# Kernel tuning notes

Hardware: AMD Instinct MI355X
Metric: run time of the kernel (lower is better)

The kernel has to match this reference:

```python
import jax, jax.numpy as jnp
import numpy as np

BN_EPS = 1e-5
L2_EPS = 1e-12  # F.normalize eps
K = 9           # kernel_size (dilation=1 so effective k = 9)
GROUPS = 4      # hard-coded groups in MRConv2d


def setup_inputs() -> dict:
    key = jax.random.key(0)
    k1, k2, k3 = jax.random.split(key, 3)
    B, C, H, W = 32, 192, 28, 28
    Cout = 384
    x = jax.random.normal(k1, (B, C, H, W), jnp.float32)
    # Conv2d(2C, Cout, 1, groups=4) weight is [Cout, 2C//4, 1, 1]; store as [Cout, 2C//4]
    fan_in = 2 * C // GROUPS
    conv_w = jax.random.normal(k2, (Cout, fan_in), jnp.float32) * np.sqrt(2.0 / fan_in)
    conv_b = jax.random.normal(k3, (Cout,), jnp.float32) * 0.05
    gamma = jnp.ones((Cout,), jnp.float32)
    beta = jnp.zeros((Cout,), jnp.float32)
    return {"x": x, "conv_w": conv_w, "conv_b": conv_b, "gamma": gamma, "beta": beta}


def _knn_idx(xf, k):
    """xf: (B, C, N) -> nn_idx: (B, N, k) via L2-normalized pairwise distance + topk."""
    xn = xf / jnp.maximum(jnp.linalg.norm(xf, axis=1, keepdims=True), L2_EPS)
    xt = xn.transpose(0, 2, 1)                       # (B, N, C)
    sq = jnp.sum(xt * xt, axis=-1, keepdims=True)    # (B, N, 1)
    inner = jnp.einsum('bnc,bmc->bnm', xt, xt)       # (B, N, N)
    dist = sq - 2.0 * inner + sq.transpose(0, 2, 1)
    _, nn_idx = jax.lax.top_k(-dist, k)              # (B, N, k)
    return nn_idx


def _forward(x, conv_w, conv_b, gamma, beta):
    B, C, H, W = x.shape
    N = H * W
    xf = x.reshape(B, C, N)
    # KNN graph built on detached features (torch: no_grad + x.detach for y when r=1)
    y = jax.lax.stop_gradient(xf)
    nn_idx = _knn_idx(y, K)                                            # (B, N, K)
    # gather neighbor features: xj[b,c,n,kk] = y[b,c,nn_idx[b,n,kk]]
    xj = jax.vmap(lambda yb, ib: yb[:, ib])(y, nn_idx)                 # (B, C, N, K)
    # max-relative: max_k (x_j - x_i); center gather of edge_index[1] is just xf
    rel = jnp.max(xj - xf[:, :, :, None], axis=-1)                     # (B, C, N)
    # cat([x.unsqueeze(2), rel.unsqueeze(2)], dim=2).reshape(B, 2C, N): channel-interleaved
    h = jnp.stack([xf, rel], axis=2).reshape(B, 2 * C, N)
    # grouped 1x1 conv, groups=4
    Cin = 2 * C
    Cout = conv_w.shape[0]
    hg = h.reshape(B, GROUPS, Cin // GROUPS, N)
    wg = conv_w.reshape(GROUPS, Cout // GROUPS, Cin // GROUPS)
    out = jnp.einsum('bgin,goi->bgon', hg, wg).reshape(B, Cout, N)
    out = out + conv_b[None, :, None]
    # BatchNorm2d (training-mode batch stats, biased variance)
    mean = jnp.mean(out, axis=(0, 2), keepdims=True)
    var = jnp.var(out, axis=(0, 2), keepdims=True)
    out = (out - mean) * jax.lax.rsqrt(var + BN_EPS)
    out = out * gamma[None, :, None] + beta[None, :, None]
    # exact (erf-based) GELU, matching torch.nn.GELU default
    out = jax.nn.gelu(out, approximate=False)
    return out.reshape(B, Cout, H, W)


def reference(x, conv_w, conv_b, gamma, beta):
    return _forward(x, conv_w, conv_b, gamma, beta)
```

## Files before the change

### kernel.cpp

```cpp
#include <hip/hip_runtime.h>

#define B_    32
#define C_    192
#define N_    784
#define NP_   1024
#define K_    9
#define COUT_ 384
#define NPTS_ (B_ * N_)
#define NTILES_ 224
#define DKW_  836

typedef __attribute__((ext_vector_type(8))) short short8;
typedef __attribute__((ext_vector_type(4))) float f32x4;

__device__ __forceinline__ unsigned int ford(float f) {
  unsigned int u = __float_as_uint(f);
  return u ^ ((u & 0x80000000u) ? 0xFFFFFFFFu : 0x80000000u);
}
__device__ __forceinline__ unsigned short f2bf(float f) {
  unsigned int u = __float_as_uint(f);
  u += 0x7FFFu + ((u >> 16) & 1u);
  return (unsigned short)(u >> 16);
}
__device__ __forceinline__ float bf2f(unsigned short h) {
  return __uint_as_float(((unsigned int)h) << 16);
}

__global__ __launch_bounds__(256) void norm_kernel(
    const float* __restrict__ x, short8* __restrict__ fragH,
    short8* __restrict__ fragL, float* __restrict__ sqp) {
  int t = threadIdx.x;
  int pl = t & 63, cg = t >> 6;
  int p = blockIdx.x * 64 + pl;
  int b = p / N_, n = p % N_;
  const float* xb = x + (size_t)b * C_ * N_ + n;

  __shared__ float red[4][64];
  __shared__ float nrmS[64];

  float part = 0.f;
  #pragma unroll 8
  for (int j = 0; j < 48; j++) {
    float v = xb[(size_t)(cg * 48 + j) * N_];
    part = __fmaf_rn(v, v, part);
  }
  red[cg][pl] = part;
  __syncthreads();
  if (t < 64) {
    float ssq = __fadd_rn(__fadd_rn(red[0][t], red[1][t]),
                          __fadd_rn(red[2][t], red[3][t]));
    nrmS[t] = fmaxf(__fsqrt_rn(ssq), 1e-12f);
  }
  __syncthreads();
  float nrm = nrmS[pl];
  int g = n >> 4, li = n & 15;
  float p2 = 0.f;
  #pragma unroll
  for (int s = 0; s < 6; s++) {
    int kslot = cg * 6 + s;
    int ks = kslot >> 2, kq = kslot & 3;
    union { short8 v; unsigned short u[8]; } ph, plo;
    #pragma unroll
    for (int j = 0; j < 8; j++) {
      float a = __fdiv_rn(xb[(size_t)(kslot * 8 + j) * N_], nrm);
      unsigned short h = f2bf(a);
      ph.u[j]  = h;
      plo.u[j] = f2bf(__fsub_rn(a, bf2f(h)));
      p2 = __fmaf_rn(a, a, p2);
    }
    size_t idx = (((size_t)b * 6 + ks) * 64 + g) * 64 + (kq * 16 + li);
    fragH[idx] = ph.v;
    fragL[idx] = plo.v;
  }
  red[cg][pl] = p2;
  __syncthreads();
  if (t < 64) {
    float sq = __fadd_rn(__fadd_rn(red[0][t], red[1][t]),
                         __fadd_rn(red[2][t], red[3][t]));
    int pp = blockIdx.x * 64 + t;
    sqp[(size_t)(pp / N_) * NP_ + (pp % N_)] = sq;
  }
}

__global__ __launch_bounds__(256) void knn_kernel(
    const short8* __restrict__ fragH, const short8* __restrict__ fragL,
    const float* __restrict__ sqp, int* __restrict__ nn9) {
  int wg = blockIdx.x;
  int r = wg & 7, j = wg >> 3;
  int b  = r + 8 * (j / 49);
  int qt = j % 49;
  int q0 = qt * 16;
  int t = threadIdx.x, lane = t & 63, w = t >> 6;

  __shared__ unsigned int dkS[16][DKW_];
  __shared__ float qsqS[16];

  for (int i = t; i < 16 * 52; i += 256)
    dkS[i / 52][784 + i % 52] = 0xFFFFFFFFu;
  if (t < 16) qsqS[t] = sqp[(size_t)b * NP_ + q0 + t];
  __syncthreads();

  const float* sqb = sqp + (size_t)b * NP_;
  const short8* fH = fragH + (size_t)b * 6 * 64 * 64;
  const short8* fL = fragL + (size_t)b * 6 * 64 * 64;

  short8 aH[6], aL[6];
  #pragma unroll
  for (int ks = 0; ks < 6; ks++) {
    aH[ks] = fH[((size_t)ks * 64 + qt) * 64 + lane];
    aL[ks] = fL[((size_t)ks * 64 + qt) * 64 + lane];
  }

  int colL = lane & 15, rq = lane >> 4;
  const int wstart = (w == 0) ? 0 : (w == 1) ? 13 : (w == 2) ? 26 : 39;
  const int wend   = (w == 0) ? 13 : (w == 1) ? 26 : (w == 2) ? 39 : 49;

  int g = wstart;
  for (; g + 1 < wend; g += 2) {
    int g0 = g, g1 = g + 1;
    f32x4 a00 = {0.f, 0.f, 0.f, 0.f}, a01 = a00, a02 = a00;
    f32x4 a10 = a00, a11 = a00, a12 = a00;
    #pragma unroll
    for (int ks = 0; ks < 6; ks++) {
      short8 b0h = fH[((size_t)ks * 64 + g0) * 64 + lane];
      short8 b0l = fL[((size_t)ks * 64 + g0) * 64 + lane];
      short8 b1h = fH[((size_t)ks * 64 + g1) * 64 + lane];
      short8 b1l = fL[((size_t)ks * 64 + g1) * 64 + lane];
      a00 = __builtin_amdgcn_mfma_f32_16x16x32_bf16(aH[ks], b0h, a00, 0, 0, 0);
      a01 = __builtin_amdgcn_mfma_f32_16x16x32_bf16(aH[ks], b0l, a01, 0, 0, 0);
      a02 = __builtin_amdgcn_mfma_f32_16x16x32_bf16(aL[ks], b0h, a02, 0, 0, 0);
      a10 = __builtin_amdgcn_mfma_f32_16x16x32_bf16(aH[ks], b1h, a10, 0, 0, 0);
      a11 = __builtin_amdgcn_mfma_f32_16x16x32_bf16(aH[ks], b1l, a11, 0, 0, 0);
      a12 = __builtin_amdgcn_mfma_f32_16x16x32_bf16(aL[ks], b1h, a12, 0, 0, 0);
    }
    float cs0 = sqb[g0 * 16 + colL];
    float cs1 = sqb[g1 * 16 + colL];
    #pragma unroll
    for (int rr = 0; rr < 4; rr++) {
      int row = rq * 4 + rr;
      float qs = qsqS[row];
      float g0v = __fadd_rn(__fadd_rn(a00[rr], a01[rr]), a02[rr]);
      float g1v = __fadd_rn(__fadd_rn(a10[rr], a11[rr]), a12[rr]);
      float d0 = __fadd_rn(__fsub_rn(qs, __fmul_rn(2.0f, g0v)), cs0);
      float d1 = __fadd_rn(__fsub_rn(qs, __fmul_rn(2.0f, g1v)), cs1);
      dkS[row][g0 * 16 + colL] = ford(d0);
      dkS[row][g1 * 16 + colL] = ford(d1);
    }
  }
  if (g < wend) {
    int g0 = g;
    f32x4 a00 = {0.f, 0.f, 0.f, 0.f}, a01 = a00, a02 = a00;
    #pragma unroll
    for (int ks = 0; ks < 6; ks++) {
      short8 b0h = fH[((size_t)ks * 64 + g0) * 64 + lane];
      short8 b0l = fL[((size_t)ks * 64 + g0) * 64 + lane];
      a00 = __builtin_amdgcn_mfma_f32_16x16x32_bf16(aH[ks], b0h, a00, 0, 0, 0);
      a01 = __builtin_amdgcn_mfma_f32_16x16x32_bf16(aH[ks], b0l, a01, 0, 0, 0);
      a02 = __builtin_amdgcn_mfma_f32_16x16x32_bf16(aL[ks], b0h, a02, 0, 0, 0);
    }
    float cs0 = sqb[g0 * 16 + colL];
    #pragma unroll
    for (int rr = 0; rr < 4; rr++) {
      int row = rq * 4 + rr;
      float qs = qsqS[row];
      float g0v = __fadd_rn(__fadd_rn(a00[rr], a01[rr]), a02[rr]);
      float d0 = __fadd_rn(__fsub_rn(qs, __fmul_rn(2.0f, g0v)), cs0);
      dkS[row][g0 * 16 + colL] = ford(d0);
    }
  }
  __syncthreads();

  for (int s = 0; s < 4; s++) {
    int row = w * 4 + s;
    unsigned int bv = 0xFFFFFFFFu; int bi = lane;
    #pragma unroll
    for (int it = 0; it < 13; it++) {
      unsigned int k = dkS[row][lane + 64 * it];
      if (k < bv) { bv = k; bi = lane + 64 * it; }
    }
    int* o = nn9 + ((size_t)b * N_ + q0 + row) * K_;
    for (int kk = 0; kk < K_; kk++) {
      unsigned long long mk = ((unsigned long long)bv << 10) | (unsigned int)bi;
      #pragma unroll
      for (int off = 1; off < 64; off <<= 1) {
        unsigned long long v2 = __shfl_xor(mk, off);
        mk = v2 < mk ? v2 : mk;
      }
      int widx = (int)(mk & 1023u);
      if (lane == 0) o[kk] = widx;
      if ((widx & 63) == lane) {
        dkS[row][widx] = 0xFFFFFFFFu;
        bv = 0xFFFFFFFFu; bi = lane;
        #pragma unroll
        for (int it = 0; it < 13; it++) {
          unsigned int k = dkS[row][lane + 64 * it];
          if (k < bv) { bv = k; bi = lane + 64 * it; }
        }
      }
    }
  }
}

__global__ __launch_bounds__(256) void fconv_kernel(
    const float* __restrict__ x, const int* __restrict__ nn9,
    const float* __restrict__ w, const float* __restrict__ bias,
    float* __restrict__ outpre, float* __restrict__ psum,
    float* __restrict__ pss) {
  int nt = blockIdx.x;
  int g  = blockIdx.y;
  int b  = blockIdx.z;
  int n0 = nt * 112;
  int t = threadIdx.x;

  __shared__ float Wl[48][97];
  __shared__ float Hl[96][112];
  __shared__ unsigned short Il[112][K_];

  const int* isrc = nn9 + ((size_t)b * N_ + n0) * K_;
  for (int i = t; i < 112 * K_; i += 256)
    Il[i / K_][i % K_] = (unsigned short)isrc[i];
  const float* wsrc0 = w + (size_t)(g * 96) * 96;
  for (int i = t; i < 48 * 96; i += 256) Wl[i / 96][i % 96] = wsrc0[i];
  __syncthreads();

  const float* xb = x + (size_t)b * C_ * N_;
  for (int pos = t; pos < 48 * 112; pos += 256) {
    int cl = pos / 112, nl = pos % 112;
    const float* row = xb + (size_t)(g * 48 + cl) * N_;
    float xv = row[n0 + nl];
    float mx = -1e30f;
    #pragma unroll
    for (int k = 0; k < K_; k++) mx = fmaxf(mx, row[Il[nl][k]]);
    Hl[2 * cl][nl]     = xv;
    Hl[2 * cl + 1][nl] = mx - xv;
  }
  __syncthreads();

  int tx = t & 15, ty = t >> 4;
  int tidx = b * 7 + nt;

  for (int half = 0; half < 2; half++) {
    float o[3][7];
    #pragma unroll
    for (int i = 0; i < 3; i++)
      #pragma unroll
      for (int j = 0; j < 7; j++) o[i][j] = 0.f;

    for (int k = 0; k < 96; k++) {
      float w0 = Wl[ty * 3 + 0][k];
      float w1 = Wl[ty * 3 + 1][k];
      float w2 = Wl[ty * 3 + 2][k];
      #pragma unroll
      for (int j = 0; j < 7; j++) {
        float hv = Hl[k][tx * 7 + j];
        o[0][j] = __fmaf_rn(w0, hv, o[0][j]);
        o[1][j] = __fmaf_rn(w1, hv, o[1][j]);
        o[2][j] = __fmaf_rn(w2, hv, o[2][j]);
      }
    }

    #pragma unroll
    for (int i = 0; i < 3; i++) {
      int co = g * 96 + half * 48 + ty * 3 + i;
      float bv = bias[co];
      float s = 0.f, s2 = 0.f;
      float* orow = outpre + ((size_t)b * COUT_ + co) * N_ + n0 + tx * 7;
      #pragma unroll
      for (int j = 0; j < 7; j++) {
        float v = o[i][j] + bv;
        orow[j] = v;
        s += v; s2 += v * v;
      }
      #pragma unroll
      for (int off = 1; off < 16; off <<= 1) {
        s  += __shfl_xor(s, off);
        s2 += __shfl_xor(s2, off);
      }
      if (tx == 0) {
        psum[co * NTILES_ + tidx] = s;
        pss [co * NTILES_ + tidx] = s2;
      }
    }

    if (half == 0) {
      __syncthreads();
      const float* wsrc1 = w + (size_t)(g * 96 + 48) * 96;
      for (int i = t; i < 48 * 96; i += 256) Wl[i / 96][i % 96] = wsrc1[i];
      __syncthreads();
    }
  }
}

__global__ __launch_bounds__(64) void stats_kernel(
    const float* __restrict__ psum, const float* __restrict__ pss,
    const float* __restrict__ gamma, const float* __restrict__ beta,
    float* __restrict__ af, float* __restrict__ bf) {
  int co = blockIdx.x;
  int l = threadIdx.x;
  double s = 0.0, s2 = 0.0;
  for (int i = l; i < NTILES_; i += 64) {
    s  += (double)psum[co * NTILES_ + i];
    s2 += (double)pss [co * NTILES_ + i];
  }
  #pragma unroll
  for (int o = 32; o > 0; o >>= 1) { s += __shfl_xor(s, o); s2 += __shfl_xor(s2, o); }
  if (l == 0) {
    const double cnt = (double)NPTS_;
    double mean = s / cnt;
    double var  = s2 / cnt - mean * mean;
    double rstd = 1.0 / sqrt(var + 1e-5);
    double a = (double)gamma[co] * rstd;
    af[co] = (float)a;
    bf[co] = (float)((double)beta[co] - mean * a);
  }
}

__global__ __launch_bounds__(256) void act_kernel(
    const float* __restrict__ outpre, const float* __restrict__ af,
    const float* __restrict__ bf, float* __restrict__ out) {
  size_t i = ((size_t)blockIdx.x * 256 + threadIdx.x) * 4;
  int co = (int)((i / N_) % COUT_);
  float a = af[co], c = bf[co];
  float4 v = *(const float4*)(outpre + i);
  float y0 = a * v.x + c, y1 = a * v.y + c, y2 = a * v.z + c, y3 = a * v.w + c;
  const float is2 = 0.70710678118654752f;
  float4 r;
  r.x = 0.5f * y0 * (1.0f + erff(y0 * is2));
  r.y = 0.5f * y1 * (1.0f + erff(y1 * is2));
  r.z = 0.5f * y2 * (1.0f + erff(y2 * is2));
  r.w = 0.5f * y3 * (1.0f + erff(y3 * is2));
  *reinterpret_cast<float4*>(out + i) = r;
}

extern "C" void kernel_launch(void* const* d_in, const int* in_sizes, int n_in,
                              void* d_out, int out_size, void* d_ws, size_t ws_size,
                              hipStream_t stream) {
  const float* x      = (const float*)d_in[0];
  const float* conv_w = (const float*)d_in[1];
  const float* conv_b = (const float*)d_in[2];
  const float* gamma  = (const float*)d_in[3];
  const float* beta   = (const float*)d_in[4];
  float* out = (float*)d_out;

  float* buf0 = (float*)d_ws;
  short8* fragH = (short8*)buf0;
  short8* fragL = (short8*)(buf0 + 3145728);
  float*  sqp   = buf0 + 6291456;
  int*    nn9   = (int*)(buf0 + 6324224);
  float*  outpre = buf0 + 6550016;
  float*  psum  = buf0 + 16183808;
  float*  pss   = psum + COUT_ * NTILES_;
  float*  af    = pss + COUT_ * NTILES_;
  float*  bfv   = af + COUT_;

  hipLaunchKernelGGL(norm_kernel, dim3(NPTS_ / 64), dim3(256), 0, stream,
                     x, fragH, fragL, sqp);
  hipLaunchKernelGGL(knn_kernel, dim3(49 * B_), dim3(256), 0, stream,
                     fragH, fragL, sqp, nn9);
  hipLaunchKernelGGL(fconv_kernel, dim3(7, 4, B_), dim3(256), 0, stream,
                     x, nn9, conv_w, conv_b, outpre, psum, pss);
  hipLaunchKernelGGL(stats_kernel, dim3(COUT_), dim3(64), 0, stream,
                     psum, pss, gamma, beta, af, bfv);
  hipLaunchKernelGGL(act_kernel, dim3((B_ * COUT_ * N_) / (256 * 4)), dim3(256), 0, stream,
                     outpre, af, bfv, out);
}
```

Measured before the change: 209.6 us.

## Process 32 query rows per KNN block to reuse key fragments across two query tiles

The KNN kernel now handles two 16-row query tiles per workgroup with 512 threads (8 waves), so each loaded key fragment feeds twice as many MFMAs. The grid shrinks from 49 to 25 query tiles per batch, and the last tile is clamped, with rows past N skipped in selection. This halves global key-fragment traffic per query, at the cost of doubled LDS (32x836 words), more accumulator registers and possibly lower occupancy.

Measured after the change: 227.0 us. 8.3% more time.

```diff
diff --git a/kernel.cpp b/kernel.cpp
--- a/kernel.cpp
+++ b/kernel.cpp
@@ -82,96 +82,125 @@
   }
 }
 
-__global__ __launch_bounds__(256) void knn_kernel(
+__global__ __launch_bounds__(512) void knn_kernel(
     const short8* __restrict__ fragH, const short8* __restrict__ fragL,
     const float* __restrict__ sqp, int* __restrict__ nn9) {
   int wg = blockIdx.x;
   int r = wg & 7, j = wg >> 3;
-  int b  = r + 8 * (j / 49);
-  int qt = j % 49;
-  int q0 = qt * 16;
+  int b  = r + 8 * (j / 25);
+  int qt = j % 25;
+  int q0 = qt * 32;
   int t = threadIdx.x, lane = t & 63, w = t >> 6;
 
-  __shared__ unsigned int dkS[16][DKW_];
-  __shared__ float qsqS[16];
-
-  for (int i = t; i < 16 * 52; i += 256)
+  __shared__ unsigned int dkS[32][DKW_];
+  __shared__ float qsqS[32];
+
+  for (int i = t; i < 32 * 52; i += 512)
     dkS[i / 52][784 + i % 52] = 0xFFFFFFFFu;
-  if (t < 16) qsqS[t] = sqp[(size_t)b * NP_ + q0 + t];
+  if (t < 32) qsqS[t] = sqp[(size_t)b * NP_ + q0 + t];
   __syncthreads();
 
   const float* sqb = sqp + (size_t)b * NP_;
   const short8* fH = fragH + (size_t)b * 6 * 64 * 64;
   const short8* fL = fragL + (size_t)b * 6 * 64 * 64;
 
-  short8 aH[6], aL[6];
+  int ga0 = qt * 2;
+  int ga1 = (qt * 2 + 1 > 48) ? 48 : (qt * 2 + 1);
+
+  short8 aH0[6], aL0[6], aH1[6], aL1[6];
   #pragma unroll
   for (int ks = 0; ks < 6; ks++) {
-    aH[ks] = fH[((size_t)ks * 64 + qt) * 64 + lane];
-    aL[ks] = fL[((size_t)ks * 64 + qt) * 64 + lane];
+    aH0[ks] = fH[((size_t)ks * 64 + ga0) * 64 + lane];
+    aL0[ks] = fL[((size_t)ks * 64 + ga0) * 64 + lane];
+    aH1[ks] = fH[((size_t)ks * 64 + ga1) * 64 + lane];
+    aL1[ks] = fL[((size_t)ks * 64 + ga1) * 64 + lane];
   }
 
   int colL = lane & 15, rq = lane >> 4;
-  const int wstart = (w == 0) ? 0 : (w == 1) ? 13 : (w == 2) ? 26 : 39;
-  const int wend   = (w == 0) ? 13 : (w == 1) ? 26 : (w == 2) ? 39 : 49;
+  int wstart = (w == 0) ? 0 : 7 + (w - 1) * 6;
+  int wend   = wstart + ((w == 0) ? 7 : 6);
 
   int g = wstart;
   for (; g + 1 < wend; g += 2) {
     int g0 = g, g1 = g + 1;
-    f32x4 a00 = {0.f, 0.f, 0.f, 0.f}, a01 = a00, a02 = a00;
-    f32x4 a10 = a00, a11 = a00, a12 = a00;
+    f32x4 z = {0.f, 0.f, 0.f, 0.f};
+    f32x4 c00h = z, c00l = z, c00x = z, c01h = z, c01l = z, c01x = z;
+    f32x4 c10h = z, c10l = z, c10x = z, c11h = z, c11l = z, c11x = z;
     #pragma unroll
     for (int ks = 0; ks < 6; ks++) {
       short8 b0h = fH[((size_t)ks * 64 + g0) * 64 + lane];
       short8 b0l = fL[((size_t)ks * 64 + g0) * 64 + lane];
       short8 b1h = fH[((size_t)ks * 64 + g1) * 64 + lane];
       short8 b1l = fL[((size_t)ks * 64 + g1) * 64 + lane];
-      a00 = __builtin_amdgcn_mfma_f32_16x16x32_bf16(aH[ks], b0h, a00, 0, 0, 0);
-      a01 = __builtin_amdgcn_mfma_f32_16x16x32_bf16(aH[ks], b0l, a01, 0, 0, 0);
-      a02 = __builtin_amdgcn_mfma_f32_16x16x32_bf16(aL[ks], b0h, a02, 0, 0, 0);
-      a10 = __builtin_amdgcn_mfma_f32_16x16x32_bf16(aH[ks], b1h, a10, 0, 0, 0);
-      a11 = __builtin_amdgcn_mfma_f32_16x16x32_bf16(aH[ks], b1l, a11, 0, 0, 0);
-      a12 = __builtin_amdgcn_mfma_f32_16x16x32_bf16(aL[ks], b1h, a12, 0, 0, 0);
+      c00h = __builtin_amdgcn_mfma_f32_16x16x32_bf16(aH0[ks], b0h, c00h, 0, 0, 0);
+      c00l = __builtin_amdgcn_mfma_f32_16x16x32_bf16(aH0[ks], b0l, c00l, 0, 0, 0);
+      c00x = __builtin_amdgcn_mfma_f32_16x16x32_bf16(aL0[ks], b0h, c00x, 0, 0, 0);
+      c01h = __builtin_amdgcn_mfma_f32_16x16x32_bf16(aH0[ks], b1h, c01h, 0, 0, 0);
+      c01l = __builtin_amdgcn_mfma_f32_16x16x32_bf16(aH0[ks], b1l, c01l, 0, 0, 0);
+      c01x = __builtin_amdgcn_mfma_f32_16x16x32_bf16(aL0[ks], b1h, c01x, 0, 0, 0);
+      c10h = __builtin_amdgcn_mfma_f32_16x16x32_bf16(aH1[ks], b0h, c10h, 0, 0, 0);
+      c10l = __builtin_amdgcn_mfma_f32_16x16x32_bf16(aH1[ks], b0l, c10l, 0, 0, 0);
+      c10x = __builtin_amdgcn_mfma_f32_16x16x32_bf16(aL1[ks], b0h, c10x, 0, 0, 0);
+      c11h = __builtin_amdgcn_mfma_f32_16x16x32_bf16(aH1[ks], b1h, c11h, 0, 0, 0);
+      c11l = __builtin_amdgcn_mfma_f32_16x16x32_bf16(aH1[ks], b1l, c11l, 0, 0, 0);
+      c11x = __builtin_amdgcn_mfma_f32_16x16x32_bf16(aL1[ks], b1h, c11x, 0, 0, 0);
     }
     float cs0 = sqb[g0 * 16 + colL];
     float cs1 = sqb[g1 * 16 + colL];
     #pragma unroll
     for (int rr = 0; rr < 4; rr++) {
       int row = rq * 4 + rr;
-      float qs = qsqS[row];
-      float g0v = __fadd_rn(__fadd_rn(a00[rr], a01[rr]), a02[rr]);
-      float g1v = __fadd_rn(__fadd_rn(a10[rr], a11[rr]), a12[rr]);
-      float d0 = __fadd_rn(__fsub_rn(qs, __fmul_rn(2.0f, g0v)), cs0);
-      float d1 = __fadd_rn(__fsub_rn(qs, __fmul_rn(2.0f, g1v)), cs1);
-      dkS[row][g0 * 16 + colL] = ford(d0);
-      dkS[row][g1 * 16 + colL] = ford(d1);
+      float qs0 = qsqS[row];
+      float g0v = __fadd_rn(__fadd_rn(c00h[rr], c00l[rr]), c00x[rr]);
+      float g1v = __fadd_rn(__fadd_rn(c01h[rr], c01l[rr]), c01x[rr]);
+      dkS[row][g0 * 16 + colL] =
+          ford(__fadd_rn(__fsub_rn(qs0, __fmul_rn(2.0f, g0v)), cs0));
+      dkS[row][g1 * 16 + colL] =
+          ford(__fadd_rn(__fsub_rn(qs0, __fmul_rn(2.0f, g1v)), cs1));
+      float qs1 = qsqS[16 + row];
+      float h0v = __fadd_rn(__fadd_rn(c10h[rr], c10l[rr]), c10x[rr]);
+      float h1v = __fadd_rn(__fadd_rn(c11h[rr], c11l[rr]), c11x[rr]);
+      dkS[16 + row][g0 * 16 + colL] =
+          ford(__fadd_rn(__fsub_rn(qs1, __fmul_rn(2.0f, h0v)), cs0));
+      dkS[16 + row][g1 * 16 + colL] =
+          ford(__fadd_rn(__fsub_rn(qs1, __fmul_rn(2.0f, h1v)), cs1));
     }
   }
   if (g < wend) {
     int g0 = g;
-    f32x4 a00 = {0.f, 0.f, 0.f, 0.f}, a01 = a00, a02 = a00;
+    f32x4 z = {0.f, 0.f, 0.f, 0.f};
+    f32x4 c00h = z, c00l = z, c00x = z;
+    f32x4 c10h = z, c10l = z, c10x = z;
     #pragma unroll
     for (int ks = 0; ks < 6; ks++) {
       short8 b0h = fH[((size_t)ks * 64 + g0) * 64 + lane];
       short8 b0l = fL[((size_t)ks * 64 + g0) * 64 + lane];
-      a00 = __builtin_amdgcn_mfma_f32_16x16x32_bf16(aH[ks], b0h, a00, 0, 0, 0);
-      a01 = __builtin_amdgcn_mfma_f32_16x16x32_bf16(aH[ks], b0l, a01, 0, 0, 0);
-      a02 = __builtin_amdgcn_mfma_f32_16x16x32_bf16(aL[ks], b0h, a02, 0, 0, 0);
+      c00h = __builtin_amdgcn_mfma_f32_16x16x32_bf16(aH0[ks], b0h, c00h, 0, 0, 0);
+      c00l = __builtin_amdgcn_mfma_f32_16x16x32_bf16(aH0[ks], b0l, c00l, 0, 0, 0);
+      c00x = __builtin_amdgcn_mfma_f32_16x16x32_bf16(aL0[ks], b0h, c00x, 0, 0, 0);
+      c10h = __builtin_amdgcn_mfma_f32_16x16x32_bf16(aH1[ks], b0h, c10h, 0, 0, 0);
+      c10l = __builtin_amdgcn_mfma_f32_16x16x32_bf16(aH1[ks], b0l, c10l, 0, 0, 0);
+      c10x = __builtin_amdgcn_mfma_f32_16x16x32_bf16(aL1[ks], b0h, c10x, 0, 0, 0);
     }
     float cs0 = sqb[g0 * 16 + colL];
     #pragma unroll
     for (int rr = 0; rr < 4; rr++) {
       int row = rq * 4 + rr;
-      float qs = qsqS[row];
-      float g0v = __fadd_rn(__fadd_rn(a00[rr], a01[rr]), a02[rr]);
-      float d0 = __fadd_rn(__fsub_rn(qs, __fmul_rn(2.0f, g0v)), cs0);
-      dkS[row][g0 * 16 + colL] = ford(d0);
+      float qs0 = qsqS[row];
+      float g0v = __fadd_rn(__fadd_rn(c00h[rr], c00l[rr]), c00x[rr]);
+      dkS[row][g0 * 16 + colL] =
+          ford(__fadd_rn(__fsub_rn(qs0, __fmul_rn(2.0f, g0v)), cs0));
+      float qs1 = qsqS[16 + row];
+      float h0v = __fadd_rn(__fadd_rn(c10h[rr], c10l[rr]), c10x[rr]);
+      dkS[16 + row][g0 * 16 + colL] =
+          ford(__fadd_rn(__fsub_rn(qs1, __fmul_rn(2.0f, h0v)), cs0));
     }
   }
   __syncthreads();
 
   for (int s = 0; s < 4; s++) {
     int row = w * 4 + s;
+    if (q0 + row >= N_) continue;
     unsigned int bv = 0xFFFFFFFFu; int bi = lane;
     #pragma unroll
     for (int it = 0; it < 13; it++) {
@@ -355,7 +384,7 @@
 
   hipLaunchKernelGGL(norm_kernel, dim3(NPTS_ / 64), dim3(256), 0, stream,
                      x, fragH, fragL, sqp);
-  hipLaunchKernelGGL(knn_kernel, dim3(49 * B_), dim3(256), 0, stream,
+  hipLaunchKernelGGL(knn_kernel, dim3(25 * B_), dim3(512), 0, stream,
                      fragH, fragL, sqp, nn9);
   hipLaunchKernelGGL(fconv_kernel, dim3(7, 4, B_), dim3(256), 0, stream,
                      x, nn9, conv_w, conv_b, outpre, psum, pss);
```
